# Kernel optimization log

Measured on AMD Instinct MI355X. Metric: run time of the kernel, lower is better.

Reference implementation:

```python
import jax, jax.numpy as jnp
import numpy as np

B, H, W, C = 4, 64, 64, 64


def _self_atten(x, q_w, q_b, v_w, v_b, dim):
    # x: [B, N, dim]; torch Linear weight is [out, in] -> x @ W.T + b
    q = jnp.einsum('bnd,od->bno', x, q_w) + q_b
    k = q  # original module uses q_linear for both q and k
    v = jnp.einsum('bnd,od->bno', x, v_w) + v_b
    a = jax.nn.sigmoid(jnp.einsum('bnd,bmd->bnm', q, k) / jnp.sqrt(jnp.float32(dim)))
    return jnp.einsum('bnm,bmd->bnd', a, v)


def setup_inputs() -> dict:
    key = jax.random.key(0)
    ks = jax.random.split(key, 11)
    s = 0.05
    return {
        'x': jax.random.normal(ks[0], (B, H, W, C), jnp.float32),
        'hq_w': jax.random.normal(ks[1], (H, H), jnp.float32) * s,
        'hq_b': jax.random.normal(ks[2], (H,), jnp.float32) * s,
        'hv_w': jax.random.normal(ks[3], (H, H), jnp.float32) * s,
        'hv_b': jax.random.normal(ks[4], (H,), jnp.float32) * s,
        'wq_w': jax.random.normal(ks[5], (W, W), jnp.float32) * s,
        'wq_b': jax.random.normal(ks[6], (W,), jnp.float32) * s,
        'wv_w': jax.random.normal(ks[7], (W, W), jnp.float32) * s,
        'wv_b': jax.random.normal(ks[8], (W,), jnp.float32) * s,
        'h_weight': jax.random.normal(ks[9], (1,), jnp.float32) * s,
        'w_weight': jax.random.normal(ks[10], (1,), jnp.float32) * s,
    }


def reference(x, hq_w, hq_b, hv_w, hv_b, wq_w, wq_b, wv_w, wv_b, h_weight, w_weight):
    b, h, w, c = x.shape
    # height axis attention: seq = W*C, feature dim = H
    xh = jnp.transpose(x, (0, 2, 3, 1)).reshape(b, w * c, h)
    xh = _self_atten(xh, hq_w, hq_b, hv_w, hv_b, h)
    xh = jnp.transpose(xh.reshape(b, w, c, h), (0, 3, 1, 2))  # [B,H,W,C]
    x = xh * h_weight + x
    # width axis attention: seq = H*C, feature dim = W
    xw = jnp.transpose(x, (0, 1, 3, 2)).reshape(b, h * c, w)
    xw = _self_atten(xw, wq_w, wq_b, wv_w, wv_b, w)
    xw = jnp.transpose(xw.reshape(b, h, c, w), (0, 1, 3, 2))  # [B,H,W,C]
    x = xw * w_weight + x
    return x
```

## Files before the change

### kernel.cpp

```cpp
#include <hip/hip_runtime.h>
#include <hip/hip_bf16.h>
#include <hip/hip_fp8.h>


typedef __attribute__((ext_vector_type(8)))  short        short8;
typedef __attribute__((ext_vector_type(16))) float        f32x16;
typedef __attribute__((ext_vector_type(4)))  unsigned int u32x4;
typedef __attribute__((ext_vector_type(2)))  unsigned int u32x2;
typedef __attribute__((ext_vector_type(4)))  float        f32x4;
union u4l { u32x4 v; long l[2]; };

#define BHWC (4096 * 64)
#define ALPHA 0.35355339f

__device__ __forceinline__ unsigned short f2bf(float f) {
    __hip_bfloat16 h = __float2bfloat16(f);
    union { __hip_bfloat16 h; unsigned short u; } c; c.h = h;
    return c.u;
}
__device__ __forceinline__ unsigned char f2fp8(float f) {
    __hip_fp8_e4m3 h(f);
    return (unsigned char)h.__x;
}
__device__ __forceinline__ float sigpoly(float z) {
    return __builtin_fmaf(z, __builtin_fmaf(z * z, -0.020833333f, 0.25f), 0.5f);
}
__device__ __forceinline__ f32x16 zero16() {
    f32x16 z;
    #pragma unroll
    for (int r = 0; r < 16; ++r) z[r] = 0.0f;
    return z;
}

__global__ __launch_bounds__(256) void wprep_kernel(
    const float* __restrict__ Wq1, const float* __restrict__ Wv1,
    const float* __restrict__ Wq2, const float* __restrict__ Wv2,
    unsigned short* __restrict__ wf)
{
    const int j = blockIdx.x * 256 + threadIdx.x;
    const int e = j & 7;
    int t = j >> 3;
    const int l31 = t & 31; t >>= 5;
    const int hi  = t & 1;  t >>= 1;
    const int dc  = t & 3;  t >>= 2;
    const int nc  = t & 1;  t >>= 1;
    const int mat = t & 1;  t >>= 1;
    const int pass = t;
    const int o = nc * 32 + l31;
    const int d = dc * 16 + hi * 8 + e;
    const float* W = pass ? (mat ? Wv2 : Wq2) : (mat ? Wv1 : Wq1);
    const float w = W[o * 64 + d] * (mat ? 1.0f : ALPHA);
    wf[j] = f2bf(w);
}

template<int MODE>
__global__ __launch_bounds__(256) void proj_kernel(
    const float* __restrict__ xsrc,
    const float* __restrict__ Bq, const float* __restrict__ Bv,
    const unsigned short* __restrict__ wf,
    unsigned char* __restrict__ Qo8, unsigned short* __restrict__ VTo)
{
    __shared__ __align__(16) unsigned short xbf[32 * 64];
    __shared__ __align__(16) unsigned char  qst8[2048];
    __shared__ __align__(16) unsigned short vst[2048];

    const int b = blockIdx.x >> 7, tile = blockIdx.x & 127, n0 = tile << 5;
    const int tid = threadIdx.x;
    const float* xb = xsrc + b * BHWC;

    for (int i = tid; i < 2048; i += 256) {
        const int d = i >> 5, nl = i & 31;
        float v;
        if (MODE == 0) v = xb[d * 4096 + n0 + nl];
        else           v = xb[(tile >> 1) * 4096 + d * 64 + (tile & 1) * 32 + nl];
        xbf[nl * 64 + (d ^ ((nl & 7) << 3))] = f2bf(v);
    }
    __syncthreads();

    const int wave = tid >> 6, lane = tid & 63, l31 = lane & 31, hi = lane >> 5;
    const int mat = wave >> 1, nc = wave & 1;
    const int o = nc * 32 + l31;

    const unsigned short* wfb = wf + (mat * 2 + nc) * 2048 + hi * 256 + l31 * 8;
    f32x16 acc = zero16();
    #pragma unroll
    for (int dc = 0; dc < 4; ++dc) {
        const short8 a  = *(const short8*)&xbf[l31 * 64 + ((dc * 16 + hi * 8) ^ ((l31 & 7) << 3))];
        const short8 bw = *(const short8*)(wfb + dc * 512);
        acc = __builtin_amdgcn_mfma_f32_32x32x16_bf16(a, bw, acc, 0, 0, 0);
    }
    const float bias = mat ? Bv[o] : (Bq[o] * ALPHA);

    if (mat == 0) {
        const int qidx = ((o >> 5) << 10) + (((o >> 3) & 1) << 9)
                       + (((o >> 4) & 1) << 3) + (o & 7);
        #pragma unroll
        for (int reg = 0; reg < 16; ++reg) {
            const int nl = (reg & 3) + 8 * (reg >> 2) + 4 * hi;
            qst8[qidx + nl * 16] = f2fp8(acc[reg] + bias);
        }
    } else {
        #pragma unroll
        for (int reg = 0; reg < 16; ++reg) {
            const int nl = (reg & 3) + 8 * (reg >> 2) + 4 * hi;
            vst[nc * 1024 + ((nl >> 4) << 9) + (((nl >> 3) & 1) << 8) + l31 * 8 + (nl & 7)]
                = f2bf(acc[reg] + bias);
        }
    }
    __syncthreads();

    {
        unsigned char*  Qg = Qo8 + b * BHWC + tile * 2048;
        unsigned short* Vg = VTo + b * BHWC + tile * 1024;
        if (tid < 128)
            *(u32x4*)(Qg + tid * 16) = *(const u32x4*)(qst8 + tid * 16);
        const int c = tid;
        const int d0 = c >> 7, r = c & 127;
        *(u32x4*)(Vg + d0 * 131072 + r * 8) = *(const u32x4*)(vst + c * 8);
    }
}

template<int MODE>
__global__ __launch_bounds__(512, 4) void attn_kernel(
    const unsigned char*  __restrict__ Q8,
    const unsigned short* __restrict__ VT,
    const float* __restrict__ xres,
    const float* __restrict__ wsc,
    float* __restrict__ xout)
{
    __shared__ __align__(16) char smem[2 * 8 * 4608];
    float* Obuf = (float*)smem;

    const int raw = (int)blockIdx.x;
    const int L = (raw & 7) * 64 + (raw >> 3);
    const int b = L >> 7, mt = L & 127;
    const int tid = threadIdx.x, wave = tid >> 6, lane = tid & 63;
    const int l31 = lane & 31, hi = lane >> 5;
    const int kq = wave;
    const unsigned char*  Q8b = Q8 + (long)b * BHWC;
    const unsigned short* Vb  = VT + b * BHWC;

    char* const bufA = smem + wave * 4608;
    char* const bufB = smem + 36864 + wave * 4608;
    const int wboff = l31 * 144 + 8 * hi;
    const int proff = l31 * 144 + 16 * hi;

    const unsigned char* qp = Q8b + mt * 2048 + hi * 512 + l31 * 16;
    u4l qA, qB;
    qA.v = *(const u32x4*)(qp);
    qB.v = *(const u32x4*)(qp + 1024);
    const long qfl0 = qA.l[0], qfl1 = qA.l[1], qfl2 = qB.l[0], qfl3 = qB.l[1];

    f32x16 acc[2]; acc[0] = zero16(); acc[1] = zero16();

    auto SIGSTORE = [&](const f32x16& s, char* dst) {
        #pragma unroll
        for (int q = 0; q < 4; ++q) {
            const float p0 = sigpoly(s[4 * q    ]);
            const float p1 = sigpoly(s[4 * q + 1]);
            const float p2 = sigpoly(s[4 * q + 2]);
            const float p3 = sigpoly(s[4 * q + 3]);
            u32x2 pk;
            pk[0] = (unsigned int)f2bf(p0) | ((unsigned int)f2bf(p1) << 16);
            pk[1] = (unsigned int)f2bf(p2) | ((unsigned int)f2bf(p3) << 16);
            *(u32x2*)(dst + 16 * q) = pk;
        }
    };
    auto QKSIG = [&](int i, char* bufC) {
        const unsigned char* kp = Q8b + (kq * 16 + i * 2) * 2048 + hi * 512 + l31 * 16;
        #pragma unroll
        for (int krc = 0; krc < 2; ++krc) {
            u4l kA, kB;
            kA.v = *(const u32x4*)(kp + krc * 2048);
            kB.v = *(const u32x4*)(kp + krc * 2048 + 1024);
            f32x16 s = zero16();
            s = __builtin_amdgcn_mfma_f32_32x32x16_fp8_fp8(kA.l[0], qfl0, s, 0, 0, 0);
            s = __builtin_amdgcn_mfma_f32_32x32x16_fp8_fp8(kA.l[1], qfl1, s, 0, 0, 0);
            s = __builtin_amdgcn_mfma_f32_32x32x16_fp8_fp8(kB.l[0], qfl2, s, 0, 0, 0);
            s = __builtin_amdgcn_mfma_f32_32x32x16_fp8_fp8(kB.l[1], qfl3, s, 0, 0, 0);
            SIGSTORE(s, bufC + wboff + krc * 64);
        }
    };
    auto PVmm = [&](int i, short8 pf0, short8 pf1, short8 pf2, short8 pf3) {
        const unsigned short* vp = Vb + (kq * 32 + i * 4) * 512 + hi * 256 + l31 * 8;
        short8 vf00 = *(const short8*)(vp + 0 * 512);
        short8 vf01 = *(const short8*)(vp + 0 * 512 + 131072);
        short8 vf10 = *(const short8*)(vp + 1 * 512);
        short8 vf11 = *(const short8*)(vp + 1 * 512 + 131072);
        acc[0] = __builtin_amdgcn_mfma_f32_32x32x16_bf16(pf0, vf00, acc[0], 0, 0, 0);
        acc[1] = __builtin_amdgcn_mfma_f32_32x32x16_bf16(pf0, vf01, acc[1], 0, 0, 0);
        acc[0] = __builtin_amdgcn_mfma_f32_32x32x16_bf16(pf1, vf10, acc[0], 0, 0, 0);
        acc[1] = __builtin_amdgcn_mfma_f32_32x32x16_bf16(pf1, vf11, acc[1], 0, 0, 0);
        vf00 = *(const short8*)(vp + 2 * 512);
        vf01 = *(const short8*)(vp + 2 * 512 + 131072);
        vf10 = *(const short8*)(vp + 3 * 512);
        vf11 = *(const short8*)(vp + 3 * 512 + 131072);
        acc[0] = __builtin_amdgcn_mfma_f32_32x32x16_bf16(pf2, vf00, acc[0], 0, 0, 0);
        acc[1] = __builtin_amdgcn_mfma_f32_32x32x16_bf16(pf2, vf01, acc[1], 0, 0, 0);
        acc[0] = __builtin_amdgcn_mfma_f32_32x32x16_bf16(pf3, vf10, acc[0], 0, 0, 0);
        acc[1] = __builtin_amdgcn_mfma_f32_32x32x16_bf16(pf3, vf11, acc[1], 0, 0, 0);
    };

    QKSIG(0, bufA);
    char* bc = bufB;
    char* bp = bufA;
    #pragma unroll 1
    for (int t = 1; t < 8; ++t) {
        short8 pf0 = *(const short8*)(bp + proff +  0);
        short8 pf1 = *(const short8*)(bp + proff + 32);
        short8 pf2 = *(const short8*)(bp + proff + 64);
        short8 pf3 = *(const short8*)(bp + proff + 96);
        QKSIG(t, bc);
        PVmm(t - 1, pf0, pf1, pf2, pf3);
        char* tmp = bc; bc = bp; bp = tmp;
    }
    {
        short8 pf0 = *(const short8*)(bp + proff +  0);
        short8 pf1 = *(const short8*)(bp + proff + 32);
        short8 pf2 = *(const short8*)(bp + proff + 64);
        short8 pf3 = *(const short8*)(bp + proff + 96);
        PVmm(7, pf0, pf1, pf2, pf3);
    }

    __syncthreads();
    if (wave < 4) {
        float* Ob = Obuf + wave * 2112;
        #pragma unroll
        for (int dc2 = 0; dc2 < 2; ++dc2)
            #pragma unroll
            for (int reg = 0; reg < 16; ++reg)
                Ob[(dc2 * 32 + l31) * 33 + (reg & 3) + 8 * (reg >> 2) + 4 * hi] = acc[dc2][reg];
    }
    __syncthreads();
    if (wave >= 4) {
        float* Ob = Obuf + (wave - 4) * 2112;
        #pragma unroll
        for (int dc2 = 0; dc2 < 2; ++dc2)
            #pragma unroll
            for (int reg = 0; reg < 16; ++reg)
                Ob[(dc2 * 32 + l31) * 33 + (reg & 3) + 8 * (reg >> 2) + 4 * hi] += acc[dc2][reg];
    }
    __syncthreads();

    const float w = wsc[0];
    const int d = tid >> 3, ms = (tid & 7) << 2;
    long base;
    if (MODE == 0) base = (long)b * BHWC + d * 4096 + mt * 32 + ms;
    else           base = (long)b * BHWC + (mt >> 1) * 4096 + d * 64 + (mt & 1) * 32 + ms;
    const int idx = d * 33 + ms;
    const float* O0 = Obuf + 0 * 2112 + idx;
    const float* O1 = Obuf + 1 * 2112 + idx;
    const float* O2 = Obuf + 2 * 2112 + idx;
    const float* O3 = Obuf + 3 * 2112 + idx;
    f32x4 r = *(const f32x4*)(xres + base);
    f32x4 o;
    #pragma unroll
    for (int j = 0; j < 4; ++j)
        o[j] = (O0[j] + O1[j] + O2[j] + O3[j]) * w + r[j];
    *(f32x4*)(xout + base) = o;
}

extern "C" void kernel_launch(void* const* d_in, const int* in_sizes, int n_in,
                              void* d_out, int out_size, void* d_ws, size_t ws_size,
                              hipStream_t stream) {
    const float* x    = (const float*)d_in[0];
    const float* hq_w = (const float*)d_in[1];
    const float* hq_b = (const float*)d_in[2];
    const float* hv_w = (const float*)d_in[3];
    const float* hv_b = (const float*)d_in[4];
    const float* wq_w = (const float*)d_in[5];
    const float* wq_b = (const float*)d_in[6];
    const float* wv_w = (const float*)d_in[7];
    const float* wv_b = (const float*)d_in[8];
    const float* h_wt = (const float*)d_in[9];
    const float* w_wt = (const float*)d_in[10];
    float* out = (float*)d_out;

    unsigned char*  Qws8 = (unsigned char*)d_ws;
    unsigned short* VTws = (unsigned short*)(Qws8 + 4 * BHWC);
    unsigned short* wfb  = VTws + 4 * BHWC;

    wprep_kernel<<<64, 256, 0, stream>>>(hq_w, hv_w, wq_w, wv_w, wfb);
    proj_kernel<0><<<512, 256, 0, stream>>>(x, hq_b, hv_b, wfb, Qws8, VTws);
    attn_kernel<0><<<512, 512, 0, stream>>>(Qws8, VTws, x, h_wt, out);
    proj_kernel<1><<<512, 256, 0, stream>>>(out, wq_b, wv_b, wfb + 8192, Qws8, VTws);
    attn_kernel<1><<<512, 512, 0, stream>>>(Qws8, VTws, out, w_wt, out);
}
```

Measured before the change: 66.56 us.

## Process two query tiles per attention block to reuse K and V loads

Each attention block now handles two 32-row query tiles instead of one, so every K and V fragment loaded from global memory feeds twice as many MFMAs. The grid is halved to 256 blocks and the launch bound drops to 2 blocks per CU so each thread can hold four accumulators. The QK/PV software pipeline is removed: each iteration computes both sigmoid tiles, then runs PV, with no double buffering. This trades lower occupancy and less overlap for half the K/V load traffic, and the epilogue stores 8 floats per thread.

```diff
diff --git a/kernel.cpp b/kernel.cpp
--- a/kernel.cpp
+++ b/kernel.cpp
@@ -121,37 +121,43 @@
 }
 
 template<int MODE>
-__global__ __launch_bounds__(512, 4) void attn_kernel(
+__global__ __launch_bounds__(512, 2) void attn_kernel(
     const unsigned char*  __restrict__ Q8,
     const unsigned short* __restrict__ VT,
     const float* __restrict__ xres,
     const float* __restrict__ wsc,
     float* __restrict__ xout)
 {
-    __shared__ __align__(16) char smem[2 * 8 * 4608];
+    __shared__ __align__(16) char smem[16 * 4608];
     float* Obuf = (float*)smem;
 
     const int raw = (int)blockIdx.x;
-    const int L = (raw & 7) * 64 + (raw >> 3);
-    const int b = L >> 7, mt = L & 127;
+    const int L = (raw & 7) * 32 + (raw >> 3);
+    const int b = L >> 6, mt = L & 63;
     const int tid = threadIdx.x, wave = tid >> 6, lane = tid & 63;
     const int l31 = lane & 31, hi = lane >> 5;
     const int kq = wave;
     const unsigned char*  Q8b = Q8 + (long)b * BHWC;
     const unsigned short* Vb  = VT + b * BHWC;
 
-    char* const bufA = smem + wave * 4608;
-    char* const bufB = smem + 36864 + wave * 4608;
+    char* const Pw0 = smem + (wave * 2 + 0) * 4608;
+    char* const Pw1 = smem + (wave * 2 + 1) * 4608;
     const int wboff = l31 * 144 + 8 * hi;
     const int proff = l31 * 144 + 16 * hi;
 
-    const unsigned char* qp = Q8b + mt * 2048 + hi * 512 + l31 * 16;
-    u4l qA, qB;
-    qA.v = *(const u32x4*)(qp);
-    qB.v = *(const u32x4*)(qp + 1024);
-    const long qfl0 = qA.l[0], qfl1 = qA.l[1], qfl2 = qB.l[0], qfl3 = qB.l[1];
-
-    f32x16 acc[2]; acc[0] = zero16(); acc[1] = zero16();
+    long qf0[4], qf1[4];
+    {
+        const unsigned char* qp0 = Q8b + (mt * 2 + 0) * 2048 + hi * 512 + l31 * 16;
+        const unsigned char* qp1 = Q8b + (mt * 2 + 1) * 2048 + hi * 512 + l31 * 16;
+        u4l a, c, d, e;
+        a.v = *(const u32x4*)(qp0);        c.v = *(const u32x4*)(qp0 + 1024);
+        d.v = *(const u32x4*)(qp1);        e.v = *(const u32x4*)(qp1 + 1024);
+        qf0[0] = a.l[0]; qf0[1] = a.l[1]; qf0[2] = c.l[0]; qf0[3] = c.l[1];
+        qf1[0] = d.l[0]; qf1[1] = d.l[1]; qf1[2] = e.l[0]; qf1[3] = e.l[1];
+    }
+
+    f32x16 acc00, acc01, acc10, acc11;
+    acc00 = zero16(); acc01 = zero16(); acc10 = zero16(); acc11 = zero16();
 
     auto SIGSTORE = [&](const f32x16& s, char* dst) {
         #pragma unroll
@@ -166,98 +172,128 @@
             *(u32x2*)(dst + 16 * q) = pk;
         }
     };
-    auto QKSIG = [&](int i, char* bufC) {
-        const unsigned char* kp = Q8b + (kq * 16 + i * 2) * 2048 + hi * 512 + l31 * 16;
-        #pragma unroll
-        for (int krc = 0; krc < 2; ++krc) {
-            u4l kA, kB;
-            kA.v = *(const u32x4*)(kp + krc * 2048);
-            kB.v = *(const u32x4*)(kp + krc * 2048 + 1024);
+
+    #pragma unroll 1
+    for (int t = 0; t < 8; ++t) {
+        const unsigned char* kp = Q8b + (kq * 16 + t * 2) * 2048 + hi * 512 + l31 * 16;
+
+        u4l kA, kB;
+        kA.v = *(const u32x4*)(kp);
+        kB.v = *(const u32x4*)(kp + 1024);
+        {
             f32x16 s = zero16();
-            s = __builtin_amdgcn_mfma_f32_32x32x16_fp8_fp8(kA.l[0], qfl0, s, 0, 0, 0);
-            s = __builtin_amdgcn_mfma_f32_32x32x16_fp8_fp8(kA.l[1], qfl1, s, 0, 0, 0);
-            s = __builtin_amdgcn_mfma_f32_32x32x16_fp8_fp8(kB.l[0], qfl2, s, 0, 0, 0);
-            s = __builtin_amdgcn_mfma_f32_32x32x16_fp8_fp8(kB.l[1], qfl3, s, 0, 0, 0);
-            SIGSTORE(s, bufC + wboff + krc * 64);
-        }
-    };
-    auto PVmm = [&](int i, short8 pf0, short8 pf1, short8 pf2, short8 pf3) {
-        const unsigned short* vp = Vb + (kq * 32 + i * 4) * 512 + hi * 256 + l31 * 8;
-        short8 vf00 = *(const short8*)(vp + 0 * 512);
-        short8 vf01 = *(const short8*)(vp + 0 * 512 + 131072);
-        short8 vf10 = *(const short8*)(vp + 1 * 512);
-        short8 vf11 = *(const short8*)(vp + 1 * 512 + 131072);
-        acc[0] = __builtin_amdgcn_mfma_f32_32x32x16_bf16(pf0, vf00, acc[0], 0, 0, 0);
-        acc[1] = __builtin_amdgcn_mfma_f32_32x32x16_bf16(pf0, vf01, acc[1], 0, 0, 0);
-        acc[0] = __builtin_amdgcn_mfma_f32_32x32x16_bf16(pf1, vf10, acc[0], 0, 0, 0);
-        acc[1] = __builtin_amdgcn_mfma_f32_32x32x16_bf16(pf1, vf11, acc[1], 0, 0, 0);
-        vf00 = *(const short8*)(vp + 2 * 512);
-        vf01 = *(const short8*)(vp + 2 * 512 + 131072);
-        vf10 = *(const short8*)(vp + 3 * 512);
-        vf11 = *(const short8*)(vp + 3 * 512 + 131072);
-        acc[0] = __builtin_amdgcn_mfma_f32_32x32x16_bf16(pf2, vf00, acc[0], 0, 0, 0);
-        acc[1] = __builtin_amdgcn_mfma_f32_32x32x16_bf16(pf2, vf01, acc[1], 0, 0, 0);
-        acc[0] = __builtin_amdgcn_mfma_f32_32x32x16_bf16(pf3, vf10, acc[0], 0, 0, 0);
-        acc[1] = __builtin_amdgcn_mfma_f32_32x32x16_bf16(pf3, vf11, acc[1], 0, 0, 0);
-    };
-
-    QKSIG(0, bufA);
-    char* bc = bufB;
-    char* bp = bufA;
-    #pragma unroll 1
-    for (int t = 1; t < 8; ++t) {
-        short8 pf0 = *(const short8*)(bp + proff +  0);
-        short8 pf1 = *(const short8*)(bp + proff + 32);
-        short8 pf2 = *(const short8*)(bp + proff + 64);
-        short8 pf3 = *(const short8*)(bp + proff + 96);
-        QKSIG(t, bc);
-        PVmm(t - 1, pf0, pf1, pf2, pf3);
-        char* tmp = bc; bc = bp; bp = tmp;
-    }
-    {
-        short8 pf0 = *(const short8*)(bp + proff +  0);
-        short8 pf1 = *(const short8*)(bp + proff + 32);
-        short8 pf2 = *(const short8*)(bp + proff + 64);
-        short8 pf3 = *(const short8*)(bp + proff + 96);
-        PVmm(7, pf0, pf1, pf2, pf3);
+            s = __builtin_amdgcn_mfma_f32_32x32x16_fp8_fp8(kA.l[0], qf0[0], s, 0, 0, 0);
+            s = __builtin_amdgcn_mfma_f32_32x32x16_fp8_fp8(kA.l[1], qf0[1], s, 0, 0, 0);
+            s = __builtin_amdgcn_mfma_f32_32x32x16_fp8_fp8(kB.l[0], qf0[2], s, 0, 0, 0);
+            s = __builtin_amdgcn_mfma_f32_32x32x16_fp8_fp8(kB.l[1], qf0[3], s, 0, 0, 0);
+            SIGSTORE(s, Pw0 + wboff);
+            s = zero16();
+            s = __builtin_amdgcn_mfma_f32_32x32x16_fp8_fp8(kA.l[0], qf1[0], s, 0, 0, 0);
+            s = __builtin_amdgcn_mfma_f32_32x32x16_fp8_fp8(kA.l[1], qf1[1], s, 0, 0, 0);
+            s = __builtin_amdgcn_mfma_f32_32x32x16_fp8_fp8(kB.l[0], qf1[2], s, 0, 0, 0);
+            s = __builtin_amdgcn_mfma_f32_32x32x16_fp8_fp8(kB.l[1], qf1[3], s, 0, 0, 0);
+            SIGSTORE(s, Pw1 + wboff);
+        }
+        kA.v = *(const u32x4*)(kp + 2048);
+        kB.v = *(const u32x4*)(kp + 3072);
+        {
+            f32x16 s = zero16();
+            s = __builtin_amdgcn_mfma_f32_32x32x16_fp8_fp8(kA.l[0], qf0[0], s, 0, 0, 0);
+            s = __builtin_amdgcn_mfma_f32_32x32x16_fp8_fp8(kA.l[1], qf0[1], s, 0, 0, 0);
+            s = __builtin_amdgcn_mfma_f32_32x32x16_fp8_fp8(kB.l[0], qf0[2], s, 0, 0, 0);
+            s = __builtin_amdgcn_mfma_f32_32x32x16_fp8_fp8(kB.l[1], qf0[3], s, 0, 0, 0);
+            SIGSTORE(s, Pw0 + wboff + 64);
+            s = zero16();
+            s = __builtin_amdgcn_mfma_f32_32x32x16_fp8_fp8(kA.l[0], qf1[0], s, 0, 0, 0);
+            s = __builtin_amdgcn_mfma_f32_32x32x16_fp8_fp8(kA.l[1], qf1[1], s, 0, 0, 0);
+            s = __builtin_amdgcn_mfma_f32_32x32x16_fp8_fp8(kB.l[0], qf1[2], s, 0, 0, 0);
+            s = __builtin_amdgcn_mfma_f32_32x32x16_fp8_fp8(kB.l[1], qf1[3], s, 0, 0, 0);
+            SIGSTORE(s, Pw1 + wboff + 64);
+        }
+
+        const unsigned short* vp = Vb + (kq * 32 + t * 4) * 512 + hi * 256 + l31 * 8;
+        const short8 vf00 = *(const short8*)(vp + 0 * 512);
+        const short8 vf01 = *(const short8*)(vp + 0 * 512 + 131072);
+        const short8 vf10 = *(const short8*)(vp + 1 * 512);
+        const short8 vf11 = *(const short8*)(vp + 1 * 512 + 131072);
+        const short8 vf20 = *(const short8*)(vp + 2 * 512);
+        const short8 vf21 = *(const short8*)(vp + 2 * 512 + 131072);
+        const short8 vf30 = *(const short8*)(vp + 3 * 512);
+        const short8 vf31 = *(const short8*)(vp + 3 * 512 + 131072);
+
+        {
+            const short8 pf0 = *(const short8*)(Pw0 + proff +  0);
+            const short8 pf1 = *(const short8*)(Pw0 + proff + 32);
+            const short8 pf2 = *(const short8*)(Pw0 + proff + 64);
+            const short8 pf3 = *(const short8*)(Pw0 + proff + 96);
+            acc00 = __builtin_amdgcn_mfma_f32_32x32x16_bf16(pf0, vf00, acc00, 0, 0, 0);
+            acc01 = __builtin_amdgcn_mfma_f32_32x32x16_bf16(pf0, vf01, acc01, 0, 0, 0);
+            acc00 = __builtin_amdgcn_mfma_f32_32x32x16_bf16(pf1, vf10, acc00, 0, 0, 0);
+            acc01 = __builtin_amdgcn_mfma_f32_32x32x16_bf16(pf1, vf11, acc01, 0, 0, 0);
+            acc00 = __builtin_amdgcn_mfma_f32_32x32x16_bf16(pf2, vf20, acc00, 0, 0, 0);
+            acc01 = __builtin_amdgcn_mfma_f32_32x32x16_bf16(pf2, vf21, acc01, 0, 0, 0);
+            acc00 = __builtin_amdgcn_mfma_f32_32x32x16_bf16(pf3, vf30, acc00, 0, 0, 0);
+            acc01 = __builtin_amdgcn_mfma_f32_32x32x16_bf16(pf3, vf31, acc01, 0, 0, 0);
+        }
+        {
+            const short8 pf0 = *(const short8*)(Pw1 + proff +  0);
+            const short8 pf1 = *(const short8*)(Pw1 + proff + 32);
+            const short8 pf2 = *(const short8*)(Pw1 + proff + 64);
+            const short8 pf3 = *(const short8*)(Pw1 + proff + 96);
+            acc10 = __builtin_amdgcn_mfma_f32_32x32x16_bf16(pf0, vf00, acc10, 0, 0, 0);
+            acc11 = __builtin_amdgcn_mfma_f32_32x32x16_bf16(pf0, vf01, acc11, 0, 0, 0);
+            acc10 = __builtin_amdgcn_mfma_f32_32x32x16_bf16(pf1, vf10, acc10, 0, 0, 0);
+            acc11 = __builtin_amdgcn_mfma_f32_32x32x16_bf16(pf1, vf11, acc11, 0, 0, 0);
+            acc10 = __builtin_amdgcn_mfma_f32_32x32x16_bf16(pf2, vf20, acc10, 0, 0, 0);
+            acc11 = __builtin_amdgcn_mfma_f32_32x32x16_bf16(pf2, vf21, acc11, 0, 0, 0);
+            acc10 = __builtin_amdgcn_mfma_f32_32x32x16_bf16(pf3, vf30, acc10, 0, 0, 0);
+            acc11 = __builtin_amdgcn_mfma_f32_32x32x16_bf16(pf3, vf31, acc11, 0, 0, 0);
+        }
     }
 
     __syncthreads();
     if (wave < 4) {
-        float* Ob = Obuf + wave * 2112;
-        #pragma unroll
-        for (int dc2 = 0; dc2 < 2; ++dc2)
-            #pragma unroll
-            for (int reg = 0; reg < 16; ++reg)
-                Ob[(dc2 * 32 + l31) * 33 + (reg & 3) + 8 * (reg >> 2) + 4 * hi] = acc[dc2][reg];
+        float* Ob = Obuf + wave * 4224;
+        #pragma unroll
+        for (int reg = 0; reg < 16; ++reg) {
+            const int m = (reg & 3) + 8 * (reg >> 2) + 4 * hi;
+            Ob[(0 * 32 + l31) * 66 +  0 + m] = acc00[reg];
+            Ob[(1 * 32 + l31) * 66 +  0 + m] = acc01[reg];
+            Ob[(0 * 32 + l31) * 66 + 32 + m] = acc10[reg];
+            Ob[(1 * 32 + l31) * 66 + 32 + m] = acc11[reg];
+        }
     }
     __syncthreads();
     if (wave >= 4) {
-        float* Ob = Obuf + (wave - 4) * 2112;
-        #pragma unroll
-        for (int dc2 = 0; dc2 < 2; ++dc2)
-            #pragma unroll
-            for (int reg = 0; reg < 16; ++reg)
-                Ob[(dc2 * 32 + l31) * 33 + (reg & 3) + 8 * (reg >> 2) + 4 * hi] += acc[dc2][reg];
+        float* Ob = Obuf + (wave - 4) * 4224;
+        #pragma unroll
+        for (int reg = 0; reg < 16; ++reg) {
+            const int m = (reg & 3) + 8 * (reg >> 2) + 4 * hi;
+            Ob[(0 * 32 + l31) * 66 +  0 + m] += acc00[reg];
+            Ob[(1 * 32 + l31) * 66 +  0 + m] += acc01[reg];
+            Ob[(0 * 32 + l31) * 66 + 32 + m] += acc10[reg];
+            Ob[(1 * 32 + l31) * 66 + 32 + m] += acc11[reg];
+        }
     }
     __syncthreads();
 
     const float w = wsc[0];
-    const int d = tid >> 3, ms = (tid & 7) << 2;
+    const int d = tid >> 3, ms = (tid & 7) << 3;
     long base;
-    if (MODE == 0) base = (long)b * BHWC + d * 4096 + mt * 32 + ms;
-    else           base = (long)b * BHWC + (mt >> 1) * 4096 + d * 64 + (mt & 1) * 32 + ms;
-    const int idx = d * 33 + ms;
-    const float* O0 = Obuf + 0 * 2112 + idx;
-    const float* O1 = Obuf + 1 * 2112 + idx;
-    const float* O2 = Obuf + 2 * 2112 + idx;
-    const float* O3 = Obuf + 3 * 2112 + idx;
-    f32x4 r = *(const f32x4*)(xres + base);
-    f32x4 o;
+    if (MODE == 0) base = (long)b * BHWC + d * 4096 + mt * 64 + ms;
+    else           base = (long)b * BHWC + mt * 4096 + d * 64 + ms;
+    const int idx = d * 66 + ms;
     #pragma unroll
-    for (int j = 0; j < 4; ++j)
-        o[j] = (O0[j] + O1[j] + O2[j] + O3[j]) * w + r[j];
-    *(f32x4*)(xout + base) = o;
+    for (int half = 0; half < 2; ++half) {
+        const int o4 = idx + half * 4;
+        f32x4 r = *(const f32x4*)(xres + base + half * 4);
+        f32x4 o;
+        #pragma unroll
+        for (int j = 0; j < 4; ++j)
+            o[j] = (Obuf[o4 + j] + Obuf[4224 + o4 + j] + Obuf[8448 + o4 + j]
+                    + Obuf[12672 + o4 + j]) * w + r[j];
+        *(f32x4*)(xout + base + half * 4) = o;
+    }
 }
 
 extern "C" void kernel_launch(void* const* d_in, const int* in_sizes, int n_in,
@@ -282,7 +318,7 @@
 
     wprep_kernel<<<64, 256, 0, stream>>>(hq_w, hv_w, wq_w, wv_w, wfb);
     proj_kernel<0><<<512, 256, 0, stream>>>(x, hq_b, hv_b, wfb, Qws8, VTws);
-    attn_kernel<0><<<512, 512, 0, stream>>>(Qws8, VTws, x, h_wt, out);
+    attn_kernel<0><<<256, 512, 0, stream>>>(Qws8, VTws, x, h_wt, out);
     proj_kernel<1><<<512, 256, 0, stream>>>(out, wq_b, wv_b, wfb + 8192, Qws8, VTws);
-    attn_kernel<1><<<512, 512, 0, stream>>>(Qws8, VTws, out, w_wt, out);
-}
+    attn_kernel<1><<<256, 512, 0, stream>>>(Qws8, VTws, out, w_wt, out);
+}
```

New measurement: 66.65 us. No clear change (+0.1%).
